# Optimization experiments

Measured on AMD Instinct MI355X. Metric: run time of the kernel, lower is better.

The kernel has to match this reference:

```python
import jax, jax.numpy as jnp
import numpy as np

N_NODES = 100000
N_EDGES = 3200000
IN_C, HID_C, OUT_C = 64, 64, 32


def setup_inputs() -> dict:
    key = jax.random.key(0)
    ks = jax.random.split(key, 8)
    x = jax.random.normal(ks[0], (N_NODES, IN_C), dtype=jnp.float32)
    edge_index = jax.random.randint(ks[1], (2, N_EDGES), 0, N_NODES, dtype=jnp.int64)
    s1 = 1.0 / np.sqrt(IN_C)
    s2 = 1.0 / np.sqrt(HID_C)
    W1l = jax.random.uniform(ks[2], (IN_C, HID_C), jnp.float32, -s1, s1)
    b1l = jnp.zeros((HID_C,), jnp.float32)
    W1r = jax.random.uniform(ks[3], (IN_C, HID_C), jnp.float32, -s1, s1)
    W2l = jax.random.uniform(ks[4], (HID_C, OUT_C), jnp.float32, -s2, s2)
    b2l = jnp.zeros((OUT_C,), jnp.float32)
    W2r = jax.random.uniform(ks[5], (HID_C, OUT_C), jnp.float32, -s2, s2)
    return {"x": x, "edge_index": edge_index, "W1l": W1l, "b1l": b1l,
            "W1r": W1r, "W2l": W2l, "b2l": b2l, "W2r": W2r}


def _sage_conv(x, src, dst, Wl, bl, Wr):
    # mean-aggregate source features onto destination nodes
    msg = x[src]                                              # [E, d] gather
    summed = jax.ops.segment_sum(msg, dst, num_segments=N_NODES)
    deg = jax.ops.segment_sum(jnp.ones((src.shape[0],), x.dtype), dst,
                              num_segments=N_NODES)
    agg = summed / jnp.maximum(deg, 1.0)[:, None]             # [N, d]
    return agg @ Wl + bl + x @ Wr                             # lin_l(agg)+lin_r(x)


def reference(x, edge_index, W1l, b1l, W1r, W2l, b2l, W2r):
    src, dst = edge_index[0], edge_index[1]
    h = jax.nn.relu(_sage_conv(x, src, dst, W1l, b1l, W1r))
    # dropout is identity in eval mode
    return _sage_conv(h, src, dst, W2l, b2l, W2r)
```

## Files before the change

### kernel.cpp

```cpp
#include <hip/hip_runtime.h>
#include <hip/hip_bf16.h>

#define N_NODES 100000
#define N_EDGES 3200000
#define NBKT 391
#define BKT_CAP 10240
#define NOCT (N_NODES / 8)

typedef __hip_bfloat16 bf16;
typedef unsigned int uint;
typedef __attribute__((ext_vector_type(8))) short bf16x8;
typedef __attribute__((ext_vector_type(4))) float f32x4;

__device__ __forceinline__ float b2f(bf16 v) { return __bfloat162float(v); }

__device__ __forceinline__ float bits2f(unsigned short w) {
    union { unsigned short u; bf16 b; } c;
    c.u = w;
    return __bfloat162float(c.b);
}
__device__ __forceinline__ unsigned short f2bits(float f) {
    return (unsigned short)(__float_as_uint(f) >> 16);
}
__device__ __forceinline__ unsigned short f2bf_bits(float f) {
    bf16 b = __float2bfloat16(f);
    unsigned short u;
    __builtin_memcpy(&u, &b, 2);
    return u;
}
__device__ __forceinline__ float lo16f(uint w) { return __uint_as_float(w << 16); }
__device__ __forceinline__ float hi16f(uint w) { return __uint_as_float(w & 0xffff0000u); }

__device__ __forceinline__ int get_xcd() {
    uint v;
    asm volatile("s_getreg_b32 %0, hwreg(20, 0, 32)" : "=s"(v));
    return (int)(v & 7);
}

__device__ __forceinline__ int get_idx(const void* ei, long long pos, int is64) {
    if (is64) return (int)((const long long*)ei)[pos];
    return ((const int*)ei)[pos];
}
__device__ __forceinline__ float get_f(const void* p, long long pos, int isbf) {
    if (isbf) return b2f(((const bf16*)p)[pos]);
    return ((const float*)p)[pos];
}

__global__ void detect_kernel(const void* __restrict__ x,
                              const void* __restrict__ ei,
                              int* __restrict__ flags) {
    int lane = threadIdx.x;
    const unsigned short* xw = (const unsigned short*)x;
    float v = bits2f(xw[2 * lane]);
    bool plaus = (v == v) && fabsf(v) > 1e-3f && fabsf(v) < 1e2f;
    unsigned long long m1 = __ballot(plaus);
    const int* iw = (const int*)ei;
    bool z = (iw[2 * lane + 1] == 0);
    unsigned long long m2 = __ballot(z);
    if (lane == 0) {
        flags[0] = (__popcll(m1) >= 32) ? 1 : 0;
        flags[1] = (__popcll(m2) == 64) ? 1 : 0;
    }
}

__global__ __launch_bounds__(256) void transpose_kernel(
    const void* __restrict__ x, uint4* __restrict__ xt,
    const int* __restrict__ flags) {
    if (!flags[0]) return;
    int i = blockIdx.x * 256 + threadIdx.x;
    if (i >= N_NODES * 4) return;
    int node = i >> 2, cz = i & 3;
    const uint4* x4 = (const uint4*)x;
    uint4 a = x4[(long long)node * 8 + cz * 2];
    uint4 b = x4[(long long)node * 8 + cz * 2 + 1];
    long long o = (long long)cz * (N_NODES * 2) + (long long)node * 2;
    xt[o] = a;
    xt[o + 1] = b;
}

__global__ __launch_bounds__(256) void scatterA_kernel(
    const void* __restrict__ ei, int* __restrict__ bucket_cursor,
    uint* __restrict__ bucket_data, const int* __restrict__ flags) {
    __shared__ int lhist[NBKT];
    __shared__ int lbase[NBKT];
    int is64 = flags[1];
    int t = threadIdx.x;
    int chunk0 = blockIdx.x * 8192;
    int dreg[32];

    for (int i = t; i < NBKT; i += 256) lhist[i] = 0;
    __syncthreads();
#pragma unroll
    for (int j = 0; j < 32; j++) {
        int e = chunk0 + j * 256 + t;
        int d = -1;
        if (e < N_EDGES) {
            d = get_idx(ei, (long long)N_EDGES + e, is64);
            atomicAdd(&lhist[d >> 8], 1);
        }
        dreg[j] = d;
    }
    __syncthreads();
    for (int i = t; i < NBKT; i += 256) {
        int c = lhist[i];
        lbase[i] = c ? atomicAdd(&bucket_cursor[i], c) : 0;
        lhist[i] = 0;
    }
    __syncthreads();
#pragma unroll
    for (int j = 0; j < 32; j++) {
        int e = chunk0 + j * 256 + t;
        int d = dreg[j];
        if (d >= 0) {
            int s = get_idx(ei, e, is64);
            int b = d >> 8;
            int o = lbase[b] + atomicAdd(&lhist[b], 1);
            if (o < BKT_CAP)
                bucket_data[(long long)b * BKT_CAP + o] = ((uint)(d & 255) << 17) | (uint)s;
        }
    }
}

__global__ void scanBuckets_kernel(const int* __restrict__ cnt,
                                   int* __restrict__ base) {
    __shared__ int buf[512];
    int t = threadIdx.x;
    int v = (t < NBKT) ? cnt[t] : 0;
    buf[t] = v;
    __syncthreads();
    for (int off = 1; off < 512; off <<= 1) {
        int add = (t >= off) ? buf[t - off] : 0;
        __syncthreads();
        buf[t] += add;
        __syncthreads();
    }
    if (t < NBKT) base[t] = buf[t] - v;
}

__global__ __launch_bounds__(256) void csrB_kernel(
    const int* __restrict__ bucket_cnt, const int* __restrict__ bucket_base,
    const uint* __restrict__ bucket_data, int* __restrict__ csr_src,
    int* __restrict__ row_start) {
    __shared__ int lh[256];
    __shared__ int buf[256];
    int b = blockIdx.x;
    int t = threadIdx.x;
    int cnt = bucket_cnt[b];
    if (cnt > BKT_CAP) cnt = BKT_CAP;
    int base = bucket_base[b];
    const uint* bd = bucket_data + (long long)b * BKT_CAP;

    lh[t] = 0;
    __syncthreads();
    for (int i = t; i < cnt; i += 256) atomicAdd(&lh[bd[i] >> 17], 1);
    __syncthreads();
    int v = lh[t];
    buf[t] = v;
    __syncthreads();
    for (int off = 1; off < 256; off <<= 1) {
        int add = (t >= off) ? buf[t - off] : 0;
        __syncthreads();
        buf[t] += add;
        __syncthreads();
    }
    int excl = buf[t] - v;
    int g = (b << 8) + t;
    if (g < N_NODES) row_start[g] = base + excl;
    lh[t] = excl;
    __syncthreads();
    for (int i = t; i < cnt; i += 256) {
        uint e = bd[i];
        int o = atomicAdd(&lh[e >> 17], 1);
        csr_src[base + o] = (int)(e & 0x1FFFFu);
    }
    if (b == 0 && t == 0) row_start[N_NODES] = N_EDGES;
}

#define ACCF4(acc, v, v2)                                                        \
    acc[0] += __uint_as_float((v).x) + __uint_as_float((v2).x);                   \
    acc[1] += __uint_as_float((v).y) + __uint_as_float((v2).y);                   \
    acc[2] += __uint_as_float((v).z) + __uint_as_float((v2).z);                   \
    acc[3] += __uint_as_float((v).w) + __uint_as_float((v2).w);

__device__ __forceinline__ void slice_gather8(
    const uint* __restrict__ su, const int* __restrict__ row_start,
    const int* __restrict__ csr_src, int nb0, int g8, int c8, int lane,
    float& a0, float& a1, int& dg_out) {
    int rl = (lane <= 8) ? row_start[nb0 + lane] : 0;
    int sg = __shfl(rl, g8 >> 3, 64);
    int eg = __shfl(rl, (g8 >> 3) + 1, 64);
    int dg = eg - sg;
    int maxd = dg;
    maxd = max(maxd, __shfl_xor(maxd, 8, 64));
    maxd = max(maxd, __shfl_xor(maxd, 16, 64));
    maxd = max(maxd, __shfl_xor(maxd, 32, 64));

    float s0f = 0.0f, s1f = 0.0f;
    for (int base = 0; base < maxd; base += 8) {
        int pf = sg + base + c8;
        int sreg = (pf < eg) ? __builtin_nontemporal_load(csr_src + pf) : 0;
        int ss[8];
#pragma unroll
        for (int u = 0; u < 8; u++) ss[u] = __shfl(sreg, g8 + u, 64);
        uint wv[8];
#pragma unroll
        for (int u = 0; u < 8; u++)
            wv[u] = (base + u < dg) ? su[(ss[u] << 3) + c8] : 0u;
#pragma unroll
        for (int u = 0; u < 8; u++) {
            s0f += lo16f(wv[u]);
            s1f += hi16f(wv[u]);
        }
    }
    a0 = s0f;
    a1 = s1f;
    dg_out = dg;
}

__global__ __launch_bounds__(256) void gather1_kernel(
    const void* __restrict__ x, const uint* __restrict__ xtu,
    const int* __restrict__ row_start, const int* __restrict__ csr_src,
    bf16* __restrict__ aggbuf, int* __restrict__ gcursor,
    const int* __restrict__ flags) {
    int isbf = flags[0];
    int t = threadIdx.x;
    int lane = t & 63;
    int bid = blockIdx.x;

    if (isbf) {
        int g8 = lane & 0x38, c8 = lane & 7;
        int g = lane >> 3;
        int cz0 = (get_xcd() >> 1) & 3;
        uint* ag = (uint*)aggbuf;
        for (int k = 0; k < 4; k++) {
            int cz = (cz0 + k) & 3;
            const uint* su = xtu + (long long)cz * (N_NODES * 8);
            while (true) {
                int oct = 0;
                if (lane == 0) oct = atomicAdd(&gcursor[cz], 1);
                oct = __shfl(oct, 0, 64);
                if (oct >= NOCT) break;
                int nb0 = oct * 8;
                float a0, a1;
                int dg;
                slice_gather8(su, row_start, csr_src, nb0, g8, c8, lane,
                              a0, a1, dg);
                float inv = 1.0f / fmaxf((float)dg, 1.0f);
                uint pk = (uint)f2bf_bits(a0 * inv) |
                          ((uint)f2bf_bits(a1 * inv) << 16);
                __builtin_nontemporal_store(pk, ag + (nb0 + g) * 32 + cz * 8 + c8);
            }
        }
    } else {
        int gw = (bid * 256 + t) >> 6;
        int nwv = (gridDim.x * 256) >> 6;
        int e4 = lane >> 4, q16 = lane & 15;
        const uint4* xf = (const uint4*)x;
        for (int p = gw; p * 2 < N_NODES; p += nwv) {
            int na = p * 2, nb = p * 2 + 1;
            int sa = row_start[na], ea = row_start[na + 1];
            int sb = row_start[nb], eb = row_start[nb + 1];
            int da = ea - sa, db = eb - sb;
            int maxd = max(da, db);
            float accA[4] = {0, 0, 0, 0};
            float accB[4] = {0, 0, 0, 0};
            for (int off = 0; off < maxd; off += 16) {
                int iA0 = sa + off + e4, iA1 = iA0 + 4, iA2 = iA0 + 8, iA3 = iA0 + 12;
                int iB0 = sb + off + e4, iB1 = iB0 + 4, iB2 = iB0 + 8, iB3 = iB0 + 12;
                int sA0 = (iA0 < ea) ? csr_src[iA0] : -1;
                int sA1 = (iA1 < ea) ? csr_src[iA1] : -1;
                int sA2 = (iA2 < ea) ? csr_src[iA2] : -1;
                int sA3 = (iA3 < ea) ? csr_src[iA3] : -1;
                int sB0 = (iB0 < eb) ? csr_src[iB0] : -1;
                int sB1 = (iB1 < eb) ? csr_src[iB1] : -1;
                int sB2 = (iB2 < eb) ? csr_src[iB2] : -1;
                int sB3 = (iB3 < eb) ? csr_src[iB3] : -1;
                uint4 vA0 = {0,0,0,0}, vA1 = {0,0,0,0}, vA2 = {0,0,0,0}, vA3 = {0,0,0,0};
                uint4 vB0 = {0,0,0,0}, vB1 = {0,0,0,0}, vB2 = {0,0,0,0}, vB3 = {0,0,0,0};
                if (sA0 >= 0) vA0 = xf[sA0 * 16 + q16];
                if (sA1 >= 0) vA1 = xf[sA1 * 16 + q16];
                if (sA2 >= 0) vA2 = xf[sA2 * 16 + q16];
                if (sA3 >= 0) vA3 = xf[sA3 * 16 + q16];
                if (sB0 >= 0) vB0 = xf[sB0 * 16 + q16];
                if (sB1 >= 0) vB1 = xf[sB1 * 16 + q16];
                if (sB2 >= 0) vB2 = xf[sB2 * 16 + q16];
                if (sB3 >= 0) vB3 = xf[sB3 * 16 + q16];
                ACCF4(accA, vA0, vA1)
                ACCF4(accA, vA2, vA3)
                ACCF4(accB, vB0, vB1)
                ACCF4(accB, vB2, vB3)
            }
#pragma unroll
            for (int m = 16; m <= 32; m <<= 1)
#pragma unroll
                for (int k = 0; k < 4; k++) {
                    accA[k] += __shfl_xor(accA[k], m, 64);
                    accB[k] += __shfl_xor(accB[k], m, 64);
                }
            float avA = 0.0f, avB = 0.0f;
#pragma unroll
            for (int k = 0; k < 4; k++) {
                float vA = __shfl(accA[k], lane >> 2, 64);
                float vB = __shfl(accB[k], lane >> 2, 64);
                avA = ((lane & 3) == k) ? vA : avA;
                avB = ((lane & 3) == k) ? vB : avB;
            }
            avA *= 1.0f / fmaxf((float)da, 1.0f);
            avB *= 1.0f / fmaxf((float)db, 1.0f);
            aggbuf[(long long)na * 64 + lane] = __float2bfloat16(avA);
            aggbuf[(long long)nb * 64 + lane] = __float2bfloat16(avB);
        }
    }
}

__global__ __launch_bounds__(256) void gemm1_kernel(
    const void* __restrict__ x, const bf16* __restrict__ aggbuf,
    const void* __restrict__ W1l, const void* __restrict__ b1l,
    const void* __restrict__ W1r, const void* __restrict__ W2l,
    const void* __restrict__ b2l, const void* __restrict__ W2r,
    bf16* __restrict__ zbufT, bf16* __restrict__ rbufT,
    const int* __restrict__ flags) {
    __shared__ __align__(16) unsigned short sW1t[64][136];
    __shared__ __align__(16) unsigned short sA[64][136];
    __shared__ __align__(16) unsigned short sW2t[64][72];
    __shared__ __align__(16) unsigned short sH[64][72];
    __shared__ float sB1[64];
    __shared__ float sB2[32];

    int isbf = flags[0];
    int t = threadIdx.x;
    int n0 = blockIdx.x * 64;

    for (int i = t; i < 64 * 128; i += 256) {
        int n = i & 63, k = i >> 6;
        unsigned short v;
        if (isbf)
            v = (k < 64) ? ((const unsigned short*)W1l)[k * 64 + n]
                         : ((const unsigned short*)W1r)[(k - 64) * 64 + n];
        else
            v = f2bits((k < 64) ? ((const float*)W1l)[k * 64 + n]
                                : ((const float*)W1r)[(k - 64) * 64 + n]);
        sW1t[n][k] = v;
    }
    for (int i = t; i < 64 * 64; i += 256) {
        int n = i & 63, k = i >> 6;
        unsigned short v;
        if (isbf)
            v = (n < 32) ? ((const unsigned short*)W2l)[k * 32 + n]
                         : ((const unsigned short*)W2r)[k * 32 + (n - 32)];
        else
            v = f2bits((n < 32) ? ((const float*)W2l)[k * 32 + n]
                                : ((const float*)W2r)[k * 32 + (n - 32)]);
        sW2t[n][k] = v;
    }
    if (t < 64) sB1[t] = get_f(b1l, t, isbf);
    if (t < 32) sB2[t] = get_f(b2l, t, isbf);

    const uint4* ag4 = (const uint4*)aggbuf;
    if (isbf) {
        const uint4* x4 = (const uint4*)x;
        for (int i = t; i < 64 * 16; i += 256) {
            int m = i >> 4, c = i & 15;
            int nn = min(n0 + m, N_NODES - 1);
            uint4 v = (c < 8) ? ag4[(long long)nn * 8 + c]
                              : x4[(long long)nn * 8 + (c - 8)];
            *(uint4*)&sA[m][c * 8] = v;
        }
    } else {
        for (int i = t; i < 64 * 8; i += 256) {
            int m = i >> 3, c = i & 7;
            int nn = min(n0 + m, N_NODES - 1);
            *(uint4*)&sA[m][c * 8] = ag4[(long long)nn * 8 + c];
        }
        const float* xf = (const float*)x;
        for (int i = t; i < 64 * 64; i += 256) {
            int m = i >> 6, c = i & 63;
            int nn = min(n0 + m, N_NODES - 1);
            sA[m][64 + c] = f2bf_bits(xf[(long long)nn * 64 + c]);
        }
    }
    __syncthreads();

    int w = t >> 6, lane = t & 63;
    int mbase = w * 16;
    int q = lane >> 4, r15 = lane & 15;
    f32x4 acc1[4] = {{0,0,0,0},{0,0,0,0},{0,0,0,0},{0,0,0,0}};
#pragma unroll
    for (int ks = 0; ks < 4; ks++) {
        bf16x8 afrag = *(const bf16x8*)&sA[mbase + r15][ks * 32 + q * 8];
#pragma unroll
        for (int nt = 0; nt < 4; nt++) {
            bf16x8 bfrag = *(const bf16x8*)&sW1t[nt * 16 + r15][ks * 32 + q * 8];
            acc1[nt] = __builtin_amdgcn_mfma_f32_16x16x32_bf16(afrag, bfrag, acc1[nt], 0, 0, 0);
        }
    }
#pragma unroll
    for (int nt = 0; nt < 4; nt++) {
        int col = nt * 16 + r15;
        float bias = sB1[col];
#pragma unroll
        for (int rr = 0; rr < 4; rr++) {
            int m = mbase + q * 4 + rr;
            sH[m][col] = f2bf_bits(fmaxf(acc1[nt][rr] + bias, 0.0f));
        }
    }
    __syncthreads();

    f32x4 acc2[4] = {{0,0,0,0},{0,0,0,0},{0,0,0,0},{0,0,0,0}};
#pragma unroll
    for (int ks = 0; ks < 2; ks++) {
        bf16x8 afrag = *(const bf16x8*)&sH[mbase + r15][ks * 32 + q * 8];
#pragma unroll
        for (int nt = 0; nt < 4; nt++) {
            bf16x8 bfrag = *(const bf16x8*)&sW2t[nt * 16 + r15][ks * 32 + q * 8];
            acc2[nt] = __builtin_amdgcn_mfma_f32_16x16x32_bf16(afrag, bfrag, acc2[nt], 0, 0, 0);
        }
    }
#pragma unroll
    for (int nt = 0; nt < 4; nt++) {
        int col = nt * 16 + r15;
#pragma unroll
        for (int rr = 0; rr < 4; rr++) {
            int m = mbase + q * 4 + rr;
            int n = n0 + m;
            if (n < N_NODES) {
                float v = acc2[nt][rr];
                if (col < 32) {
                    zbufT[(long long)(col >> 4) * (N_NODES * 16) +
                          (long long)n * 16 + (col & 15)] = __float2bfloat16(v);
                } else {
                    int c2 = col - 32;
                    rbufT[(long long)(c2 >> 4) * (N_NODES * 16) +
                          (long long)n * 16 + (c2 & 15)] =
                        __float2bfloat16(v + sB2[c2]);
                }
            }
        }
    }
}

__global__ __launch_bounds__(256) void node2_kernel(
    const int* __restrict__ row_start, const int* __restrict__ csr_src,
    const uint* __restrict__ zTu, const bf16* __restrict__ rbufT,
    void* __restrict__ out, const int* __restrict__ flags) {
    int isbf = flags[0];
    int t = threadIdx.x;
    int lane = t & 63;
    int w = t >> 6;
    int bid = blockIdx.x;
    int cz = (bid & 7) >> 2;
    int wid = ((((bid >> 3) << 2) | (bid & 3)) << 2) + w;
    int nw = gridDim.x * 2;
    int g8 = lane & 0x38, c8 = lane & 7;
    int g = lane >> 3;
    const uint* su = zTu + (long long)cz * (N_NODES * 8);
    const uint* ru = (const uint*)(rbufT + (long long)cz * (N_NODES * 16));

    for (int oct = wid; oct < NOCT; oct += nw) {
        int nb0 = oct * 8;
        float a0, a1;
        int dg;
        slice_gather8(su, row_start, csr_src, nb0, g8, c8, lane, a0, a1, dg);
        float inv = 1.0f / fmaxf((float)dg, 1.0f);
        int n = nb0 + g;
        uint rb = __builtin_nontemporal_load(ru + n * 8 + c8);
        float r0 = a0 * inv + lo16f(rb);
        float r1 = a1 * inv + hi16f(rb);
        if (isbf) {
            uint pk = (uint)f2bf_bits(r0) | ((uint)f2bf_bits(r1) << 16);
            __builtin_nontemporal_store(pk, (uint*)out + n * 16 + cz * 8 + c8);
        } else {
            float* of = (float*)out;
            __builtin_nontemporal_store(r0, of + (long long)n * 32 + cz * 16 + 2 * c8);
            __builtin_nontemporal_store(r1, of + (long long)n * 32 + cz * 16 + 2 * c8 + 1);
        }
    }
}

extern "C" void kernel_launch(void* const* d_in, const int* in_sizes, int n_in,
                              void* d_out, int out_size, void* d_ws, size_t ws_size,
                              hipStream_t stream) {
    const void* x = d_in[0];
    const void* ei = d_in[1];
    const void* W1l = d_in[2];
    const void* b1l = d_in[3];
    const void* W1r = d_in[4];
    const void* W2l = d_in[5];
    const void* b2l = d_in[6];
    const void* W2r = d_in[7];

    char* ws = (char*)d_ws;
    uint* bucket_data = (uint*)ws;
    bf16* aggbuf = (bf16*)ws;
    int* csr_src = (int*)(ws + 16015424);
    int* row_start = (int*)(ws + 28815424);
    int* bucket_cursor = (int*)(ws + 29215488);
    int* bucket_base = (int*)(ws + 29217088);
    uint* xtu = (uint*)(ws + 29218688);
    bf16* zbufT = (bf16*)(ws + 29218688);
    bf16* rbufT = (bf16*)(ws + 35618688);
    int* flags = (int*)(ws + 42018688);
    int* gcursor = (int*)(ws + 42018696);

    hipMemsetAsync(bucket_cursor, 0, NBKT * 4, stream);
    hipMemsetAsync(gcursor, 0, 16, stream);

    detect_kernel<<<1, 64, 0, stream>>>(x, ei, flags);
    transpose_kernel<<<1563, 256, 0, stream>>>(x, (uint4*)xtu, flags);
    scatterA_kernel<<<NBKT, 256, 0, stream>>>(ei, bucket_cursor, bucket_data, flags);
    scanBuckets_kernel<<<1, 512, 0, stream>>>(bucket_cursor, bucket_base);
    csrB_kernel<<<NBKT, 256, 0, stream>>>(bucket_cursor, bucket_base, bucket_data,
                                          csr_src, row_start);
    gather1_kernel<<<4096, 256, 0, stream>>>(x, xtu, row_start, csr_src, aggbuf,
                                             gcursor, flags);
    gemm1_kernel<<<1563, 256, 0, stream>>>(x, aggbuf, W1l, b1l, W1r, W2l, b2l,
                                           W2r, zbufT, rbufT, flags);
    node2_kernel<<<4096, 256, 0, stream>>>(row_start, csr_src, (const uint*)zbufT,
                                           rbufT, d_out, flags);
}
```

Measured before the change: 379.9 us.

## Split layer-1 gather into two launches with static XCD-aware channel slicing

Replaces the atomic work-stealing loop over four channel slices, where each wave picked a start slice from its hardware XCD id, with a static assignment. Each of two kernel launches handles two of the four 16-channel slices. The block index picks the slice, so a group of XCDs works on one slice and that slice's feature table can stay in their L2. This removes the atomic cursor, its memset and the XCD register read, but adds a kernel launch, relies on the round-robin block-to-XCD mapping, and gives up dynamic load balancing.

```diff
diff --git a/kernel.cpp b/kernel.cpp
--- a/kernel.cpp
+++ b/kernel.cpp
@@ -30,12 +30,6 @@
 }
 __device__ __forceinline__ float lo16f(uint w) { return __uint_as_float(w << 16); }
 __device__ __forceinline__ float hi16f(uint w) { return __uint_as_float(w & 0xffff0000u); }
-
-__device__ __forceinline__ int get_xcd() {
-    uint v;
-    asm volatile("s_getreg_b32 %0, hwreg(20, 0, 32)" : "=s"(v));
-    return (int)(v & 7);
-}
 
 __device__ __forceinline__ int get_idx(const void* ei, long long pos, int is64) {
     if (is64) return (int)((const long long*)ei)[pos];
@@ -220,38 +214,33 @@
 __global__ __launch_bounds__(256) void gather1_kernel(
     const void* __restrict__ x, const uint* __restrict__ xtu,
     const int* __restrict__ row_start, const int* __restrict__ csr_src,
-    bf16* __restrict__ aggbuf, int* __restrict__ gcursor,
-    const int* __restrict__ flags) {
+    bf16* __restrict__ aggbuf, const int* __restrict__ flags, int cz_base) {
     int isbf = flags[0];
     int t = threadIdx.x;
     int lane = t & 63;
+    int w = t >> 6;
     int bid = blockIdx.x;
 
     if (isbf) {
+        int cz = cz_base + ((bid & 7) >> 2);
+        int wid = ((((bid >> 3) << 2) | (bid & 3)) << 2) + w;
+        int nw = gridDim.x * 2;
         int g8 = lane & 0x38, c8 = lane & 7;
         int g = lane >> 3;
-        int cz0 = (get_xcd() >> 1) & 3;
+        const uint* su = xtu + (long long)cz * (N_NODES * 8);
         uint* ag = (uint*)aggbuf;
-        for (int k = 0; k < 4; k++) {
-            int cz = (cz0 + k) & 3;
-            const uint* su = xtu + (long long)cz * (N_NODES * 8);
-            while (true) {
-                int oct = 0;
-                if (lane == 0) oct = atomicAdd(&gcursor[cz], 1);
-                oct = __shfl(oct, 0, 64);
-                if (oct >= NOCT) break;
-                int nb0 = oct * 8;
-                float a0, a1;
-                int dg;
-                slice_gather8(su, row_start, csr_src, nb0, g8, c8, lane,
-                              a0, a1, dg);
-                float inv = 1.0f / fmaxf((float)dg, 1.0f);
-                uint pk = (uint)f2bf_bits(a0 * inv) |
-                          ((uint)f2bf_bits(a1 * inv) << 16);
-                __builtin_nontemporal_store(pk, ag + (nb0 + g) * 32 + cz * 8 + c8);
-            }
+        for (int oct = wid; oct < NOCT; oct += nw) {
+            int nb0 = oct * 8;
+            float a0, a1;
+            int dg;
+            slice_gather8(su, row_start, csr_src, nb0, g8, c8, lane, a0, a1, dg);
+            float inv = 1.0f / fmaxf((float)dg, 1.0f);
+            uint pk = (uint)f2bf_bits(a0 * inv) |
+                      ((uint)f2bf_bits(a1 * inv) << 16);
+            __builtin_nontemporal_store(pk, ag + (nb0 + g) * 32 + cz * 8 + c8);
         }
     } else {
+        if (cz_base != 0) return;
         int gw = (bid * 256 + t) >> 6;
         int nwv = (gridDim.x * 256) >> 6;
         int e4 = lane >> 4, q16 = lane & 15;
@@ -500,10 +489,8 @@
     bf16* zbufT = (bf16*)(ws + 29218688);
     bf16* rbufT = (bf16*)(ws + 35618688);
     int* flags = (int*)(ws + 42018688);
-    int* gcursor = (int*)(ws + 42018696);
 
     hipMemsetAsync(bucket_cursor, 0, NBKT * 4, stream);
-    hipMemsetAsync(gcursor, 0, 16, stream);
 
     detect_kernel<<<1, 64, 0, stream>>>(x, ei, flags);
     transpose_kernel<<<1563, 256, 0, stream>>>(x, (uint4*)xtu, flags);
@@ -512,7 +499,9 @@
     csrB_kernel<<<NBKT, 256, 0, stream>>>(bucket_cursor, bucket_base, bucket_data,
                                           csr_src, row_start);
     gather1_kernel<<<4096, 256, 0, stream>>>(x, xtu, row_start, csr_src, aggbuf,
-                                             gcursor, flags);
+                                             flags, 0);
+    gather1_kernel<<<4096, 256, 0, stream>>>(x, xtu, row_start, csr_src, aggbuf,
+                                             flags, 2);
     gemm1_kernel<<<1563, 256, 0, stream>>>(x, aggbuf, W1l, b1l, W1r, W2l, b2l,
                                            W2r, zbufT, rbufT, flags);
     node2_kernel<<<4096, 256, 0, stream>>>(row_start, csr_src, (const uint*)zbufT,
```

Result: no change. 381.5 us (+0.4%).
